# Performance work log

Measured on AMD Instinct MI355X. Metric: run time of the kernel, lower is better.

Reference implementation:

```python
import jax, jax.numpy as jnp
import numpy as np

EPS = 1e-5
B, CIN, L = 512, 5, 1024   # batch, input channels, msp length == d_model
COUT, A, NB = 32, 13, 5    # CNN branch channels, max_atoms, num_bonds_prediction


def conv1d(x, w, pad, groups=1):
    # x: (N, C, L), w: (O, I/groups, K)
    return jax.lax.conv_general_dilated(
        x, w, window_strides=(1,), padding=[(pad, pad)],
        dimension_numbers=("NCH", "OIH", "NCH"), feature_group_count=groups)


def batchnorm(x, g, b):
    # training-mode BN over (N, L) per channel, as nn.BatchNorm1d in train()
    m = jnp.mean(x, axis=(0, 2), keepdims=True)
    v = jnp.var(x, axis=(0, 2), keepdims=True)
    return (x - m) * jax.lax.rsqrt(v + EPS) * g[None, :, None] + b[None, :, None]


def setup_inputs() -> dict:
    key = jax.random.key(0)
    ks = jax.random.split(key, 16)
    n = jax.random.normal
    inp = {
        "src": n(ks[0], (B, CIN, L), dtype=jnp.float32),
        "mask": jnp.ones((B, A), dtype=bool),
        "max_atoms": A,
        # CNN branch 1 (kernel 5) : depthwise, pointwise, BN, residual 1x1 conv
        "dw1": n(ks[1], (CIN, 1, 5), dtype=jnp.float32) * 0.2,
        "pw1": n(ks[2], (COUT, CIN, 1), dtype=jnp.float32) * 0.2,
        "g1": jnp.ones((COUT,), jnp.float32),
        "be1": jnp.zeros((COUT,), jnp.float32),
        "r1w": n(ks[3], (COUT, CIN, 1), dtype=jnp.float32) * 0.2,
        "r1b": jnp.zeros((COUT,), jnp.float32),
        # CNN branch 2 (kernel 3)
        "dw2": n(ks[4], (CIN, 1, 3), dtype=jnp.float32) * 0.2,
        "pw2": n(ks[5], (COUT, CIN, 1), dtype=jnp.float32) * 0.2,
        "g2": jnp.ones((COUT,), jnp.float32),
        "be2": jnp.zeros((COUT,), jnp.float32),
        "r2w": n(ks[6], (COUT, CIN, 1), dtype=jnp.float32) * 0.2,
        "r2b": jnp.zeros((COUT,), jnp.float32),
        # EdgeClassify2 linears: ll1 (2*COUT -> A), fl (2*L -> NB)
        "ll1w": n(ks[7], (A, 2 * COUT), dtype=jnp.float32) * 0.1,
        "ll1b": jnp.zeros((A,), jnp.float32),
        "flw": n(ks[8], (NB, 2 * L), dtype=jnp.float32) * 0.02,
        "flb": jnp.zeros((NB,), jnp.float32),
    }
    return inp


def reference(src, mask, max_atoms, dw1, pw1, g1, be1, r1w, r1b,
              dw2, pw2, g2, be2, r2w, r2b, ll1w, ll1b, flw, flb):
    # ---- CNN encoder ----
    e1 = jax.nn.relu(batchnorm(conv1d(conv1d(src, dw1, 2, groups=CIN), pw1, 0), g1, be1))
    e1 = e1 * (conv1d(src, r1w, 0) + r1b[None, :, None])
    e2 = jax.nn.relu(batchnorm(conv1d(conv1d(src, dw2, 1, groups=CIN), pw2, 0), g2, be2))
    e2 = e2 * (conv1d(src, r2w, 0) + r2b[None, :, None])
    x = jnp.concatenate([e1, e2], axis=1)          # (B, 2*COUT, L)
    # ---- EdgeClassify2 ----
    # ll1 over channel dim: (B, 2*COUT, L) -> (B, A, L)
    h = jnp.einsum("bcl,ac->bal", x, ll1w) + ll1b[None, :, None]
    # vectorized replacement of the O(A^2) python loop:
    # final_e[:, i, j] = concat(h[:, min(i,j)], h[:, max(i,j)])
    idx = jnp.arange(max_atoms)
    mn = jnp.minimum(idx[:, None], idx[None, :])   # (A, A)
    mx = jnp.maximum(idx[:, None], idx[None, :])
    final_e = jnp.concatenate([h[:, mn, :], h[:, mx, :]], axis=-1)  # (B, A, A, 2L)
    out = jnp.einsum("bijd,nd->bijn", final_e, flw) + flb           # (B, A, A, NB)
    return out
```

## Files before the change

kernel.cpp:

```cpp
#include <hip/hip_runtime.h>
#include <hip/hip_bf16.h>

#define BB 512
#define LL 1024
#define AA 13
#define NBP 5
#define NTOT (BB * LL)
#define EPSV 1e-5f

#define WS_F     192
#define WS_PART  256
#define WS_CONST 10496
#define WS_S     16384

typedef __attribute__((ext_vector_type(8))) short bhalf8;
typedef __attribute__((ext_vector_type(4))) float floatx4;

__device__ __forceinline__ unsigned int pk_bf16(float a, float b) {
    __hip_bfloat162 h = __float22bfloat162_rn(make_float2(a, b));
    union { __hip_bfloat162 h2; unsigned int u; } cv; cv.h2 = h;
    return cv.u;
}

template<int CTRL, int RM, bool BC>
__device__ __forceinline__ float dppadd(float v) {
    int t = __builtin_amdgcn_update_dpp(0, __float_as_int(v), CTRL, RM, 0xf, BC);
    return v + __int_as_float(t);
}
__device__ __forceinline__ float wave_sum(float v) {
    v = dppadd<0x111, 0xf, true >(v);
    v = dppadd<0x112, 0xf, true >(v);
    v = dppadd<0x114, 0xf, true >(v);
    v = dppadd<0x118, 0xf, true >(v);
    v = dppadd<0x142, 0xa, false>(v);
    v = dppadd<0x143, 0xc, false>(v);
    return v;
}

__global__ __launch_bounds__(256) void k_moments(
    const float* __restrict__ src,
    const float* __restrict__ dw1,
    const float* __restrict__ dw2,
    const float* __restrict__ flw,
    float* __restrict__ ws)
{
    __shared__ float red[4][40];
    __shared__ float fred[4];
    int tid = threadIdx.x;
    int gid = blockIdx.x * 256 + tid;
    int b = gid >> 7, L0 = (gid & 127) << 3;
    const float* sb = src + b * (5 * LL);

    float w1[5][5], w2[5][3];
#pragma unroll
    for (int c = 0; c < 5; c++) {
#pragma unroll
        for (int t = 0; t < 5; t++) w1[c][t] = dw1[c*5+t];
#pragma unroll
        for (int t = 0; t < 3; t++) w2[c][t] = dw2[c*3+t];
    }

    float x[5][16];
#pragma unroll
    for (int c5 = 0; c5 < 5; c5++) {
        const float* sp = sb + c5 * LL;
        float4 xa = (L0 >= 4)    ? *(const float4*)(sp + L0 - 4) : make_float4(0,0,0,0);
        float4 xb = *(const float4*)(sp + L0);
        float4 xc = *(const float4*)(sp + L0 + 4);
        float4 xd = (L0 <= 1012) ? *(const float4*)(sp + L0 + 8) : make_float4(0,0,0,0);
        x[c5][0]=xa.x; x[c5][1]=xa.y; x[c5][2]=xa.z; x[c5][3]=xa.w;
        x[c5][4]=xb.x; x[c5][5]=xb.y; x[c5][6]=xb.z; x[c5][7]=xb.w;
        x[c5][8]=xc.x; x[c5][9]=xc.y; x[c5][10]=xc.z; x[c5][11]=xc.w;
        x[c5][12]=xd.x; x[c5][13]=xd.y; x[c5][14]=xd.z; x[c5][15]=xd.w;
    }

    float acc[40];
#pragma unroll
    for (int k = 0; k < 40; k++) acc[k] = 0.f;

#pragma unroll
    for (int k = 0; k < 8; k++) {
        float d1[5], d2[5];
#pragma unroll
        for (int c5 = 0; c5 < 5; c5++) {
            d1[c5] = w1[c5][0]*x[c5][k+2] + w1[c5][1]*x[c5][k+3] + w1[c5][2]*x[c5][k+4]
                   + w1[c5][3]*x[c5][k+5] + w1[c5][4]*x[c5][k+6];
            d2[c5] = w2[c5][0]*x[c5][k+3] + w2[c5][1]*x[c5][k+4] + w2[c5][2]*x[c5][k+5];
        }
#pragma unroll
        for (int j = 0; j < 5; j++) { acc[j] += d1[j]; acc[20+j] += d2[j]; }
#pragma unroll
        for (int j = 0; j < 5; j++)
#pragma unroll
            for (int kk = j; kk < 5; kk++) {
                int idx = j*(11-j)/2 + (kk - j);
                acc[5+idx]  += d1[j]*d1[kk];
                acc[25+idx] += d2[j]*d2[kk];
            }
    }

    int lane = tid & 63, wv = tid >> 6;
#pragma unroll
    for (int k = 0; k < 40; k++) acc[k] = wave_sum(acc[k]);
    if (lane == 63) {
#pragma unroll
        for (int k = 0; k < 40; k++) red[wv][k] = acc[k];
    }
    __syncthreads();
    if (tid < 40) {
        ws[WS_PART + blockIdx.x * 40 + tid] =
            red[0][tid] + red[1][tid] + red[2][tid] + red[3][tid];
    }

    if (blockIdx.x < 10) {
        int nn = blockIdx.x;
        int n = nn < 5 ? nn : nn - 5;
        int off = nn < 5 ? 0 : LL;
        float4 v = *(const float4*)(flw + n * (2*LL) + off + tid * 4);
        float s = wave_sum(v.x + v.y + v.z + v.w);
        if (lane == 63) fred[wv] = s;
        __syncthreads();
        if (tid == 0) ws[WS_F + nn] = fred[0] + fred[1] + fred[2] + fred[3];
    }
}

__global__ __launch_bounds__(320) void k_prep(
    float* __restrict__ ws,
    const float* __restrict__ pw1, const float* __restrict__ pw2,
    const float* __restrict__ g1,  const float* __restrict__ be1,
    const float* __restrict__ g2,  const float* __restrict__ be2,
    const float* __restrict__ r1w, const float* __restrict__ r2w,
    const float* __restrict__ r1b, const float* __restrict__ r2b)
{
    __shared__ float momS[40];
    int tid = threadIdx.x;
    {
        int k = tid >> 3, sub = tid & 7;
        float v = 0.f;
#pragma unroll 8
        for (int t2 = 0; t2 < 32; t2++) v += ws[WS_PART + (sub + (t2 << 3)) * 40 + k];
        v += __shfl_xor(v, 1, 64);
        v += __shfl_xor(v, 2, 64);
        v += __shfl_xor(v, 4, 64);
        if (sub == 0) momS[k] = v;
    }
    __syncthreads();
    if (tid < 64) {
        int brc = tid >> 5, o = tid & 31;
        const float invN = 1.0f / (float)NTOT;
        const float* pw = brc ? pw2 : pw1;
        const float* rw = brc ? r2w : r1w;
        const float* s  = momS + (brc ? 20 : 0);
        const float* M  = momS + (brc ? 25 : 5);
        float pwv[5], rwv[5], md[5];
#pragma unroll
        for (int j = 0; j < 5; j++) { pwv[j] = pw[o*5+j]; rwv[j] = rw[o*5+j]; md[j] = s[j] * invN; }
        float meanY = 0.f;
#pragma unroll
        for (int j = 0; j < 5; j++) meanY += pwv[j] * md[j];
        float ey2 = 0.f;
#pragma unroll
        for (int j = 0; j < 5; j++)
#pragma unroll
            for (int k = 0; k < 5; k++) {
                int lo = j < k ? j : k, hi = j < k ? k : j;
                int idx = lo*(11-lo)/2 + (hi - lo);
                ey2 += pwv[j] * pwv[k] * (M[idx] * invN);
            }
        float varY = ey2 - meanY * meanY;
        if (varY < 0.f) varY = 0.f;
        float gg = brc ? g2[o] : g1[o];
        float bb = brc ? be2[o] : be1[o];
        float rb = brc ? r2b[o] : r1b[o];
        float sc = gg * rsqrtf(varY + EPSV);
        float sh = bb - meanY * sc;
        float* dst = ws + WS_CONST + tid * 16;
        dst[0] = pwv[0]*sc; dst[1] = pwv[1]*sc; dst[2] = pwv[2]*sc; dst[3] = pwv[3]*sc;
        dst[4] = pwv[4]*sc; dst[5] = sh;        dst[6] = rb;        dst[7] = 0.f;
        dst[8] = rwv[0];    dst[9] = rwv[1];    dst[10] = rwv[2];   dst[11] = rwv[3];
        dst[12] = rwv[4];   dst[13] = 0.f;      dst[14] = 0.f;      dst[15] = 0.f;
    }
}

__global__ __launch_bounds__(512, 4) void k_fused(
    const float* __restrict__ src,
    const float* __restrict__ dw1,
    const float* __restrict__ dw2,
    const float* __restrict__ flw,
    const float* __restrict__ ws_ro,
    float* __restrict__ ws)
{
    __shared__ __align__(16) float dvS[9216 + 64];

    int tid = threadIdx.x, bb = blockIdx.x;
    int b = bb >> 1, h = bb & 1;
    int lane = tid & 63;
    int gu = __builtin_amdgcn_readfirstlane(tid >> 6);
    int mt = gu & 3, lq = gu >> 2;
    int br = mt >> 1;

    const float* srcB = src + b * (5 * LL);
    char* base  = (char*)dvS;
    char* cbase = (char*)(dvS + 8192);

    {
        int t = tid, lg = (h << 9) + t;
        int swz = ((t >> 3) & 3) << 4;
        float d1v[5], d2v[5], s0[5];
#pragma unroll
        for (int c5 = 0; c5 < 5; c5++) {
            const float* s5 = srcB + (c5 << 10);
            float xm2 = (lg >= 2)    ? s5[lg - 2] : 0.f;
            float xm1 = (lg >= 1)    ? s5[lg - 1] : 0.f;
            float x0  = s5[lg];
            float xp1 = (lg <= 1022) ? s5[lg + 1] : 0.f;
            float xp2 = (lg <= 1021) ? s5[lg + 2] : 0.f;
            d1v[c5] = dw1[c5*5+0]*xm2 + dw1[c5*5+1]*xm1 + dw1[c5*5+2]*x0
                    + dw1[c5*5+3]*xp1 + dw1[c5*5+4]*xp2;
            d2v[c5] = dw2[c5*3+0]*xm1 + dw2[c5*3+1]*x0 + dw2[c5*3+2]*xp1;
            s0[c5] = x0;
        }
        *(float4*)(base + ((((0<<10)+(t<<1)+0) << 4) ^ swz)) = make_float4(d1v[0],d1v[1],d1v[2],d1v[3]);
        *(float4*)(base + ((((0<<10)+(t<<1)+1) << 4) ^ swz)) = make_float4(d1v[4],s0[0],s0[1],s0[2]);
        *(float4*)(base + ((((1<<10)+(t<<1)+0) << 4) ^ swz)) = make_float4(d2v[0],d2v[1],d2v[2],d2v[3]);
        *(float4*)(base + ((((1<<10)+(t<<1)+1) << 4) ^ swz)) = make_float4(d2v[4],s0[0],s0[1],s0[2]);
        *(float2*)(cbase + (t << 3)) = make_float2(s0[3], s0[4]);
    }
    __syncthreads();

    int ch = (mt << 4) + (lane & 15);
    const float* cf = ws_ro + WS_CONST + (ch << 4);
    const float4 A  = *(const float4*)cf;
    const float4 B2 = *(const float4*)(cf + 4);
    const float4 R0 = *(const float4*)(cf + 8);
    const float r4w = cf[12];

    int nB = lane & 15;
    int kg = (lane >> 4) << 3;
    const float* fbase = flw + (nB % 5) * 2048 + (nB / 5) * 1024;
    floatx4 Cacc = {0.f, 0.f, 0.f, 0.f};

#pragma unroll 1
    for (int s = 0; s < 8; ++s) {
        int lb = (lq << 8) + (s << 5) + kg;
        float4 f0 = make_float4(0,0,0,0), f1 = make_float4(0,0,0,0);
        if (nB < 10) {
            f0 = *(const float4*)(fbase + (h << 9) + lb);
            f1 = *(const float4*)(fbase + (h << 9) + lb + 4);
        }
        int sw = ((lb >> 3) & 3) << 4;
        float e[8];
#pragma unroll
        for (int i = 0; i < 8; ++i) {
            int l = lb + i;
            const float4 pa = *(const float4*)(base + ((((br<<10)+(l<<1)+0) << 4) ^ sw));
            const float4 pb = *(const float4*)(base + ((((br<<10)+(l<<1)+1) << 4) ^ sw));
            const float2 pc = *(const float2*)(cbase + (l << 3));
            float y = B2.y + A.x*pa.x + A.y*pa.y + A.z*pa.z + A.w*pa.w + B2.x*pb.x;
            float r = B2.z + R0.x*pb.y + R0.y*pb.z + R0.z*pb.w + R0.w*pc.x + r4w*pc.y;
            e[i] = fmaxf(y, 0.f) * r;
        }
        union { unsigned int u[4]; bhalf8 v; } ah, al;
#pragma unroll
        for (int j = 0; j < 4; j++) {
            unsigned int hp = pk_bf16(e[2*j], e[2*j+1]);
            float hi0 = __uint_as_float(hp << 16);
            float hi1 = __uint_as_float(hp & 0xFFFF0000u);
            ah.u[j] = hp;
            al.u[j] = pk_bf16(e[2*j] - hi0, e[2*j+1] - hi1);
        }
        float fb[8] = {f0.x, f0.y, f0.z, f0.w, f1.x, f1.y, f1.z, f1.w};
        union { unsigned int u[4]; bhalf8 v; } bh, bl;
#pragma unroll
        for (int j = 0; j < 4; j++) {
            unsigned int hp = pk_bf16(fb[2*j], fb[2*j+1]);
            float hi0 = __uint_as_float(hp << 16);
            float hi1 = __uint_as_float(hp & 0xFFFF0000u);
            bh.u[j] = hp;
            bl.u[j] = pk_bf16(fb[2*j] - hi0, fb[2*j+1] - hi1);
        }
        Cacc = __builtin_amdgcn_mfma_f32_16x16x32_bf16(ah.v, bh.v, Cacc, 0, 0, 0);
        Cacc = __builtin_amdgcn_mfma_f32_16x16x32_bf16(ah.v, bl.v, Cacc, 0, 0, 0);
        Cacc = __builtin_amdgcn_mfma_f32_16x16x32_bf16(al.v, bh.v, Cacc, 0, 0, 0);
    }

    __syncthreads();
    {
        float* part = dvS;
        int basep = (gu << 8) + ((lane >> 4) << 6) + (lane & 15);
        part[basep]      = Cacc[0];
        part[basep + 16] = Cacc[1];
        part[basep + 32] = Cacc[2];
        part[basep + 48] = Cacc[3];
    }
    __syncthreads();
    for (int idx = tid; idx < 640; idx += 512) {
        int c = idx / 10, n = idx - c * 10;
        int mt2 = c >> 4, m = c & 15;
        const float* part = (const float*)dvS;
        int o = (m << 4) + n;
        ws[WS_S + bb * 640 + idx] = part[mt2 * 256 + o] + part[(4 + mt2) * 256 + o];
    }
}

__global__ __launch_bounds__(256) void k_out(
    const float* __restrict__ ws,
    const float* __restrict__ ll1w,
    const float* __restrict__ ll1b,
    const float* __restrict__ flb,
    float* __restrict__ out)
{
    __shared__ float llT[832];
    __shared__ float S[640];
    __shared__ float PQ[130];

    int tid = threadIdx.x, b = blockIdx.x;
    for (int idx = tid; idx < 832; idx += 256) {
        int cc = idx / 13, a = idx - cc * 13;
        llT[idx] = ll1w[a * 64 + cc];
    }
    const float* s0 = ws + WS_S + (b * 2) * 640;
    const float* s1 = ws + WS_S + (b * 2 + 1) * 640;
    for (int idx = tid; idx < 640; idx += 256) S[idx] = s0[idx] + s1[idx];
    __syncthreads();

    if (tid < 130) {
        int half = tid >= 65 ? 1 : 0;
        int q = tid - half * 65;
        int a = q / 5, n = q - a * 5;
        int col = half * 5 + n;
        float v = ll1b[a] * ws[WS_F + col];
#pragma unroll 8
        for (int cc = 0; cc < 64; cc++) v += llT[cc * 13 + a] * S[cc * 10 + col];
        PQ[tid] = v;
    }
    __syncthreads();

    for (int idx = tid; idx < AA * AA * NBP; idx += 256) {
        int i = idx / 65;
        int rr = idx - i * 65;
        int j = rr / 5, n = rr - j * 5;
        int mn = i < j ? i : j, mx = i < j ? j : i;
        out[b * (AA * AA * NBP) + idx] = PQ[mn * 5 + n] + PQ[65 + mx * 5 + n] + flb[n];
    }
}

extern "C" void kernel_launch(void* const* d_in, const int* in_sizes, int n_in,
                              void* d_out, int out_size, void* d_ws, size_t ws_size,
                              hipStream_t stream) {
    const float* src  = (const float*)d_in[0];
    const float* dw1  = (const float*)d_in[3];
    const float* pw1  = (const float*)d_in[4];
    const float* g1   = (const float*)d_in[5];
    const float* be1  = (const float*)d_in[6];
    const float* r1w  = (const float*)d_in[7];
    const float* r1b  = (const float*)d_in[8];
    const float* dw2  = (const float*)d_in[9];
    const float* pw2  = (const float*)d_in[10];
    const float* g2   = (const float*)d_in[11];
    const float* be2  = (const float*)d_in[12];
    const float* r2w  = (const float*)d_in[13];
    const float* r2b  = (const float*)d_in[14];
    const float* ll1w = (const float*)d_in[15];
    const float* ll1b = (const float*)d_in[16];
    const float* flw  = (const float*)d_in[17];
    const float* flb  = (const float*)d_in[18];
    float* ws  = (float*)d_ws;
    float* out = (float*)d_out;

    k_moments<<<256, 256, 0, stream>>>(src, dw1, dw2, flw, ws);
    k_prep<<<1, 320, 0, stream>>>(ws, pw1, pw2, g1, be1, g2, be2, r1w, r2w, r1b, r2b);
    k_fused<<<BB * 2, 512, 0, stream>>>(src, dw1, dw2, flw, ws, ws);
    k_out<<<BB, 256, 0, stream>>>(ws, ll1w, ll1b, flb, out);
}
```

Measured before the change: 142.1 us.

## Fuse output kernel into main kernel and pre-split flw into bf16 hi/lo

Merges k_out into k_fused so each block handles a whole batch row (1024 positions), computing the ll1 projection and pairwise output directly instead of writing partial sums to the workspace. The flw weights are pre-split once in k_moments into truncated bf16 hi/lo arrays, padded to 16 rows, so the main loop loads ready packed B operands instead of converting every iteration. Activation splitting now uses bit truncation instead of round-to-nearest. This saves one launch and the workspace round trip, but doubles shared memory per block and halves the grid, which lowers occupancy and parallelism.

```diff
diff --git a/kernel.cpp b/kernel.cpp
--- a/kernel.cpp
+++ b/kernel.cpp
@@ -11,15 +11,18 @@
 #define WS_F     192
 #define WS_PART  256
 #define WS_CONST 10496
-#define WS_S     16384
+#define WS_FLW   16384
 
 typedef __attribute__((ext_vector_type(8))) short bhalf8;
 typedef __attribute__((ext_vector_type(4))) float floatx4;
 
-__device__ __forceinline__ unsigned int pk_bf16(float a, float b) {
-    __hip_bfloat162 h = __float22bfloat162_rn(make_float2(a, b));
-    union { __hip_bfloat162 h2; unsigned int u; } cv; cv.h2 = h;
-    return cv.u;
+__device__ __forceinline__ void trunc_pair(float e0, float e1, unsigned int& hp, unsigned int& lp) {
+    unsigned int u0 = __float_as_uint(e0), u1 = __float_as_uint(e1);
+    unsigned int h0 = u0 & 0xFFFF0000u, h1 = u1 & 0xFFFF0000u;
+    hp = (h0 >> 16) | h1;
+    float l0 = e0 - __uint_as_float(h0);
+    float l1 = e1 - __uint_as_float(h1);
+    lp = (__float_as_uint(l0) >> 16) | (__float_as_uint(l1) & 0xFFFF0000u);
 }
 
 template<int CTRL, int RM, bool BC>
@@ -117,10 +120,23 @@
         int n = nn < 5 ? nn : nn - 5;
         int off = nn < 5 ? 0 : LL;
         float4 v = *(const float4*)(flw + n * (2*LL) + off + tid * 4);
+        {
+            unsigned int hp0, lp0, hp1, lp1;
+            trunc_pair(v.x, v.y, hp0, lp0);
+            trunc_pair(v.z, v.w, hp1, lp1);
+            char* fwb = (char*)(ws + WS_FLW);
+            *(uint2*)(fwb + nn * 2048 + tid * 8)         = make_uint2(hp0, hp1);
+            *(uint2*)(fwb + 32768 + nn * 2048 + tid * 8) = make_uint2(lp0, lp1);
+        }
         float s = wave_sum(v.x + v.y + v.z + v.w);
         if (lane == 63) fred[wv] = s;
         __syncthreads();
         if (tid == 0) ws[WS_F + nn] = fred[0] + fred[1] + fred[2] + fred[3];
+    } else if (blockIdx.x < 16) {
+        int nn = blockIdx.x;
+        char* fwb = (char*)(ws + WS_FLW);
+        *(uint2*)(fwb + nn * 2048 + tid * 8)         = make_uint2(0u, 0u);
+        *(uint2*)(fwb + 32768 + nn * 2048 + tid * 8) = make_uint2(0u, 0u);
     }
 }
 
@@ -182,18 +198,21 @@
     }
 }
 
-__global__ __launch_bounds__(512, 4) void k_fused(
+__global__ __launch_bounds__(512, 2) void k_fused(
     const float* __restrict__ src,
     const float* __restrict__ dw1,
     const float* __restrict__ dw2,
-    const float* __restrict__ flw,
+    const float* __restrict__ ll1w,
+    const float* __restrict__ ll1b,
+    const float* __restrict__ flb,
     const float* __restrict__ ws_ro,
-    float* __restrict__ ws)
+    float* __restrict__ out)
 {
-    __shared__ __align__(16) float dvS[9216 + 64];
-
-    int tid = threadIdx.x, bb = blockIdx.x;
-    int b = bb >> 1, h = bb & 1;
+    __shared__ __align__(16) float dvS[18432];
+    __shared__ float llT[832];
+    __shared__ float PQ[130];
+
+    int tid = threadIdx.x, b = blockIdx.x;
     int lane = tid & 63;
     int gu = __builtin_amdgcn_readfirstlane(tid >> 6);
     int mt = gu & 3, lq = gu >> 2;
@@ -201,30 +220,33 @@
 
     const float* srcB = src + b * (5 * LL);
     char* base  = (char*)dvS;
-    char* cbase = (char*)(dvS + 8192);
-
-    {
-        int t = tid, lg = (h << 9) + t;
+    char* cbase = (char*)(dvS + 16384);
+
+    for (int t = tid; t < 1024; t += 512) {
         int swz = ((t >> 3) & 3) << 4;
         float d1v[5], d2v[5], s0[5];
 #pragma unroll
         for (int c5 = 0; c5 < 5; c5++) {
             const float* s5 = srcB + (c5 << 10);
-            float xm2 = (lg >= 2)    ? s5[lg - 2] : 0.f;
-            float xm1 = (lg >= 1)    ? s5[lg - 1] : 0.f;
-            float x0  = s5[lg];
-            float xp1 = (lg <= 1022) ? s5[lg + 1] : 0.f;
-            float xp2 = (lg <= 1021) ? s5[lg + 2] : 0.f;
+            float xm2 = (t >= 2)    ? s5[t - 2] : 0.f;
+            float xm1 = (t >= 1)    ? s5[t - 1] : 0.f;
+            float x0  = s5[t];
+            float xp1 = (t <= 1022) ? s5[t + 1] : 0.f;
+            float xp2 = (t <= 1021) ? s5[t + 2] : 0.f;
             d1v[c5] = dw1[c5*5+0]*xm2 + dw1[c5*5+1]*xm1 + dw1[c5*5+2]*x0
                     + dw1[c5*5+3]*xp1 + dw1[c5*5+4]*xp2;
             d2v[c5] = dw2[c5*3+0]*xm1 + dw2[c5*3+1]*x0 + dw2[c5*3+2]*xp1;
             s0[c5] = x0;
         }
-        *(float4*)(base + ((((0<<10)+(t<<1)+0) << 4) ^ swz)) = make_float4(d1v[0],d1v[1],d1v[2],d1v[3]);
-        *(float4*)(base + ((((0<<10)+(t<<1)+1) << 4) ^ swz)) = make_float4(d1v[4],s0[0],s0[1],s0[2]);
-        *(float4*)(base + ((((1<<10)+(t<<1)+0) << 4) ^ swz)) = make_float4(d2v[0],d2v[1],d2v[2],d2v[3]);
-        *(float4*)(base + ((((1<<10)+(t<<1)+1) << 4) ^ swz)) = make_float4(d2v[4],s0[0],s0[1],s0[2]);
+        *(float4*)(base + ((((0<<11)+(t<<1)+0) << 4) ^ swz)) = make_float4(d1v[0],d1v[1],d1v[2],d1v[3]);
+        *(float4*)(base + ((((0<<11)+(t<<1)+1) << 4) ^ swz)) = make_float4(d1v[4],s0[0],s0[1],s0[2]);
+        *(float4*)(base + ((((1<<11)+(t<<1)+0) << 4) ^ swz)) = make_float4(d2v[0],d2v[1],d2v[2],d2v[3]);
+        *(float4*)(base + ((((1<<11)+(t<<1)+1) << 4) ^ swz)) = make_float4(d2v[4],s0[0],s0[1],s0[2]);
         *(float2*)(cbase + (t << 3)) = make_float2(s0[3], s0[4]);
+    }
+    for (int idx = tid; idx < 832; idx += 512) {
+        int cc = idx / 13, a = idx - cc * 13;
+        llT[idx] = ll1w[a * 64 + cc];
     }
     __syncthreads();
 
@@ -237,24 +259,22 @@
 
     int nB = lane & 15;
     int kg = (lane >> 4) << 3;
-    const float* fbase = flw + (nB % 5) * 2048 + (nB / 5) * 1024;
+    const char* fwb = (const char*)(ws_ro + WS_FLW);
     floatx4 Cacc = {0.f, 0.f, 0.f, 0.f};
 
 #pragma unroll 1
-    for (int s = 0; s < 8; ++s) {
-        int lb = (lq << 8) + (s << 5) + kg;
-        float4 f0 = make_float4(0,0,0,0), f1 = make_float4(0,0,0,0);
-        if (nB < 10) {
-            f0 = *(const float4*)(fbase + (h << 9) + lb);
-            f1 = *(const float4*)(fbase + (h << 9) + lb + 4);
-        }
+    for (int s = 0; s < 16; ++s) {
+        int lb = (lq << 9) + (s << 5) + kg;
+        union { uint4 u; bhalf8 v; } bh, bl;
+        bh.u = *(const uint4*)(fwb + (((nB << 10) + lb) << 1));
+        bl.u = *(const uint4*)(fwb + 32768 + (((nB << 10) + lb) << 1));
         int sw = ((lb >> 3) & 3) << 4;
         float e[8];
 #pragma unroll
         for (int i = 0; i < 8; ++i) {
             int l = lb + i;
-            const float4 pa = *(const float4*)(base + ((((br<<10)+(l<<1)+0) << 4) ^ sw));
-            const float4 pb = *(const float4*)(base + ((((br<<10)+(l<<1)+1) << 4) ^ sw));
+            const float4 pa = *(const float4*)(base + ((((br<<11)+(l<<1)+0) << 4) ^ sw));
+            const float4 pb = *(const float4*)(base + ((((br<<11)+(l<<1)+1) << 4) ^ sw));
             const float2 pc = *(const float2*)(cbase + (l << 3));
             float y = B2.y + A.x*pa.x + A.y*pa.y + A.z*pa.z + A.w*pa.w + B2.x*pb.x;
             float r = B2.z + R0.x*pb.y + R0.y*pb.z + R0.z*pb.w + R0.w*pc.x + r4w*pc.y;
@@ -262,23 +282,7 @@
         }
         union { unsigned int u[4]; bhalf8 v; } ah, al;
 #pragma unroll
-        for (int j = 0; j < 4; j++) {
-            unsigned int hp = pk_bf16(e[2*j], e[2*j+1]);
-            float hi0 = __uint_as_float(hp << 16);
-            float hi1 = __uint_as_float(hp & 0xFFFF0000u);
-            ah.u[j] = hp;
-            al.u[j] = pk_bf16(e[2*j] - hi0, e[2*j+1] - hi1);
-        }
-        float fb[8] = {f0.x, f0.y, f0.z, f0.w, f1.x, f1.y, f1.z, f1.w};
-        union { unsigned int u[4]; bhalf8 v; } bh, bl;
-#pragma unroll
-        for (int j = 0; j < 4; j++) {
-            unsigned int hp = pk_bf16(fb[2*j], fb[2*j+1]);
-            float hi0 = __uint_as_float(hp << 16);
-            float hi1 = __uint_as_float(hp & 0xFFFF0000u);
-            bh.u[j] = hp;
-            bl.u[j] = pk_bf16(fb[2*j] - hi0, fb[2*j+1] - hi1);
-        }
+        for (int j = 0; j < 4; j++) trunc_pair(e[2*j], e[2*j+1], ah.u[j], al.u[j]);
         Cacc = __builtin_amdgcn_mfma_f32_16x16x32_bf16(ah.v, bh.v, Cacc, 0, 0, 0);
         Cacc = __builtin_amdgcn_mfma_f32_16x16x32_bf16(ah.v, bl.v, Cacc, 0, 0, 0);
         Cacc = __builtin_amdgcn_mfma_f32_16x16x32_bf16(al.v, bh.v, Cacc, 0, 0, 0);
@@ -294,34 +298,14 @@
         part[basep + 48] = Cacc[3];
     }
     __syncthreads();
-    for (int idx = tid; idx < 640; idx += 512) {
-        int c = idx / 10, n = idx - c * 10;
+    float* SarrF = dvS + 4096;
+    for (int idx = tid; idx < 1024; idx += 512) {
+        int c = idx >> 4, n = idx & 15;
         int mt2 = c >> 4, m = c & 15;
         const float* part = (const float*)dvS;
         int o = (m << 4) + n;
-        ws[WS_S + bb * 640 + idx] = part[mt2 * 256 + o] + part[(4 + mt2) * 256 + o];
-    }
-}
-
-__global__ __launch_bounds__(256) void k_out(
-    const float* __restrict__ ws,
-    const float* __restrict__ ll1w,
-    const float* __restrict__ ll1b,
-    const float* __restrict__ flb,
-    float* __restrict__ out)
-{
-    __shared__ float llT[832];
-    __shared__ float S[640];
-    __shared__ float PQ[130];
-
-    int tid = threadIdx.x, b = blockIdx.x;
-    for (int idx = tid; idx < 832; idx += 256) {
-        int cc = idx / 13, a = idx - cc * 13;
-        llT[idx] = ll1w[a * 64 + cc];
-    }
-    const float* s0 = ws + WS_S + (b * 2) * 640;
-    const float* s1 = ws + WS_S + (b * 2 + 1) * 640;
-    for (int idx = tid; idx < 640; idx += 256) S[idx] = s0[idx] + s1[idx];
+        SarrF[idx] = part[mt2 * 256 + o] + part[(4 + mt2) * 256 + o];
+    }
     __syncthreads();
 
     if (tid < 130) {
@@ -329,14 +313,14 @@
         int q = tid - half * 65;
         int a = q / 5, n = q - a * 5;
         int col = half * 5 + n;
-        float v = ll1b[a] * ws[WS_F + col];
+        float v = ll1b[a] * ws_ro[WS_F + col];
 #pragma unroll 8
-        for (int cc = 0; cc < 64; cc++) v += llT[cc * 13 + a] * S[cc * 10 + col];
+        for (int cc = 0; cc < 64; cc++) v += llT[cc * 13 + a] * SarrF[(cc << 4) + col];
         PQ[tid] = v;
     }
     __syncthreads();
 
-    for (int idx = tid; idx < AA * AA * NBP; idx += 256) {
+    for (int idx = tid; idx < AA * AA * NBP; idx += 512) {
         int i = idx / 65;
         int rr = idx - i * 65;
         int j = rr / 5, n = rr - j * 5;
@@ -370,6 +354,5 @@
 
     k_moments<<<256, 256, 0, stream>>>(src, dw1, dw2, flw, ws);
     k_prep<<<1, 320, 0, stream>>>(ws, pw1, pw2, g1, be1, g2, be2, r1w, r2w, r1b, r2b);
-    k_fused<<<BB * 2, 512, 0, stream>>>(src, dw1, dw2, flw, ws, ws);
-    k_out<<<BB, 256, 0, stream>>>(ws, ll1w, ll1b, flb, out);
-}
+    k_fused<<<BB, 512, 0, stream>>>(src, dw1, dw2, ll1w, ll1b, flb, ws, out);
+}
```

Result: faster. 134.1 us (-5.6%).
